# Optimization experiments

Hardware: AMD Instinct MI355X
Metric: run time of the kernel (lower is better)

## Reference

```python
import jax, jax.numpy as jnp
import numpy as np

B, S, E, H = 2, 2048, 768, 8
D = E // H  # 96
SCALING = D ** (-0.5)


def setup_inputs() -> dict:
    key = jax.random.key(0)
    ks = jax.random.split(key, 7)
    sd = E ** -0.5
    return {
        "x": jax.random.normal(ks[0], (B, S, E), jnp.float32),
        "Wq": jax.random.normal(ks[1], (E, E), jnp.float32) * sd,
        "bq": jax.random.normal(ks[2], (E,), jnp.float32) * 0.02,
        "Wk": jax.random.normal(ks[3], (E, E), jnp.float32) * sd,
        "bk": jax.random.normal(ks[4], (E,), jnp.float32) * 0.02,
        "Wo": jax.random.normal(ks[5], (E, E), jnp.float32) * sd,
        "bo": jax.random.normal(ks[6], (E,), jnp.float32) * 0.02,
    }


def _split_heads(t):
    # [B, S, E] -> [B, H, S, D]
    return t.reshape(B, S, H, D).transpose(0, 2, 1, 3)


def reference(x, Wq, bq, Wk, bk, Wo, bo):
    q = _split_heads(x @ Wq + bq)
    k = _split_heads(x @ Wk + bk)
    # NOTE: faithful to source bug — values use the KEY projection
    v = _split_heads(x @ Wk + bk)
    energies = jnp.einsum("bhqd,bhkd->bhqk", q, k)  # [B,H,S,S]
    # NOTE: faithful to source — scaling applied AFTER softmax
    attn = jax.nn.softmax(energies, axis=-1) * SCALING
    out = jnp.einsum("bhqk,bhkd->bhqd", attn, v)
    out = out.transpose(0, 2, 1, 3).reshape(B, S, E)
    return out @ Wo + bo
```

## Files before the change

kernel.cpp:

```cpp
#include <hip/hip_runtime.h>
#include <hip/hip_bf16.h>
#include <math.h>
#include <stdint.h>

#define B_DIM 2
#define S_DIM 2048
#define E_DIM 768
#define H_DIM 8
#define D_DIM 96
#define M_DIM (B_DIM*S_DIM)
#define SCALE_F 0.10206207261596575f
#define LOG2E_F 1.44269504088896341f

typedef _Float16 f16x8 __attribute__((ext_vector_type(8)));
typedef float    f32x4  __attribute__((ext_vector_type(4)));
typedef float    f32x16 __attribute__((ext_vector_type(16)));
typedef unsigned int u32x4 __attribute__((ext_vector_type(4)));

#define MFMA16H(a,b,c) __builtin_amdgcn_mfma_f32_16x16x32_f16(a,b,c,0,0,0)
#define MFMA32H(a,b,c) __builtin_amdgcn_mfma_f32_32x32x16_f16(a,b,c,0,0,0)

__device__ inline unsigned short f2h(float f) {
    return __builtin_bit_cast(unsigned short, (_Float16)f);
}

__device__ inline unsigned pk2(float a, float b) {
    return __builtin_bit_cast(unsigned, __builtin_amdgcn_cvt_pkrtz(a, b));
}

__device__ inline void gload16(const void* g, void* l) {
    auto gp = reinterpret_cast<const __attribute__((address_space(1))) uint32_t*>(
        reinterpret_cast<uintptr_t>(g));
    auto lp = reinterpret_cast<__attribute__((address_space(3))) uint32_t*>(
        reinterpret_cast<uintptr_t>(l));
    __builtin_amdgcn_global_load_lds(gp, lp, 16, 0, 0);
}

__global__ __launch_bounds__(256) void prep_kernel(
    const float* __restrict__ X,
    const float* __restrict__ W0, const float* __restrict__ W1,
    const float* __restrict__ W2,
    unsigned short* __restrict__ Xf,
    unsigned short* __restrict__ T0, unsigned short* __restrict__ T1,
    unsigned short* __restrict__ T2)
{
    const int tid = threadIdx.x;
    if (blockIdx.x < 3072) {
        int i = (blockIdx.x * 256 + tid) * 4;
        float4 v = *(const float4*)(X + i);
        ushort4 h;
        h.x = f2h(v.x); h.y = f2h(v.y); h.z = f2h(v.z); h.w = f2h(v.w);
        *(ushort4*)(Xf + i) = h;
        return;
    }
    int idx = blockIdx.x - 3072;
    int z = idx / 144, rem = idx % 144;
    const float* W; unsigned short* T;
    if (z == 0)      { W = W0; T = T0; }
    else if (z == 1) { W = W1; T = T1; }
    else             { W = W2; T = T2; }
    const float sc = (z == 0) ? LOG2E_F : 1.0f;
    int k0 = (rem / 12) << 6, n0 = (rem % 12) << 6;

    __shared__ float tile[64][65];
    const int r = tid >> 4, c4 = (tid & 15) << 2;
    #pragma unroll
    for (int i = 0; i < 4; ++i) {
        float4 v = *(const float4*)(W + (size_t)(k0 + r + i*16)*E_DIM + n0 + c4);
        tile[r + i*16][c4+0] = v.x; tile[r + i*16][c4+1] = v.y;
        tile[r + i*16][c4+2] = v.z; tile[r + i*16][c4+3] = v.w;
    }
    __syncthreads();
    #pragma unroll
    for (int i = 0; i < 4; ++i) {
        int n = r + i*16;
        ushort4 h;
        h.x = f2h(tile[c4+0][n] * sc); h.y = f2h(tile[c4+1][n] * sc);
        h.z = f2h(tile[c4+2][n] * sc); h.w = f2h(tile[c4+3][n] * sc);
        *(ushort4*)(T + (size_t)(n0 + n)*E_DIM + k0 + c4) = h;
    }
}

__global__ __launch_bounds__(256) void gemm_qk_kernel(
    const unsigned short* __restrict__ A, const unsigned short* __restrict__ Bt,
    const float* __restrict__ bq, const float* __restrict__ bk,
    unsigned short* __restrict__ Qf, unsigned short* __restrict__ Kf)
{
    __shared__ unsigned short sA[2*128*32];
    __shared__ unsigned short sB[2*64*32];

    const int tid  = threadIdx.x;
    const int lane = tid & 63;
    const int w    = tid >> 6;
    const int qn   = lane & 15, quad = lane >> 4;
    const int wm   = w & 1, wn = w >> 1;

    const int flat = blockIdx.x;
    const int g = flat & 7, s = flat >> 3;
    const int row0 = ((g << 2) + (s & 3)) << 7;
    const int col0 = (s >> 2) << 6;

    const int ar = tid >> 2;
    const int ak = (tid & 3) << 3;

    const unsigned short* gA = A  + (size_t)(row0 + ar)*E_DIM + ak;
    const unsigned short* gB = Bt + (size_t)(col0 + ar)*E_DIM + ak;

    f32x4 acc[4][2];
    #pragma unroll
    for (int mt = 0; mt < 4; ++mt)
        #pragma unroll
        for (int nt = 0; nt < 2; ++nt)
            { acc[mt][nt][0]=0.f; acc[mt][nt][1]=0.f; acc[mt][nt][2]=0.f; acc[mt][nt][3]=0.f; }

    for (int k0 = 0; k0 < E_DIM; k0 += 64) {
        __syncthreads();
        gload16(gA + k0,                 sA + tid*8);
        gload16(gA + 64*E_DIM + k0,      sA + 2048 + tid*8);
        gload16(gA + k0 + 32,            sA + 4096 + tid*8);
        gload16(gA + 64*E_DIM + k0 + 32, sA + 6144 + tid*8);
        gload16(gB + k0,                 sB + tid*8);
        gload16(gB + k0 + 32,            sB + 2048 + tid*8);
        __syncthreads();

        #pragma unroll
        for (int kk = 0; kk < 2; ++kk) {
            f16x8 af[4], bf[2];
            #pragma unroll
            for (int mt = 0; mt < 4; ++mt)
                af[mt] = *(const f16x8*)&sA[kk*4096 + (wm*64 + mt*16 + qn)*32 + quad*8];
            #pragma unroll
            for (int nt = 0; nt < 2; ++nt)
                bf[nt] = *(const f16x8*)&sB[kk*2048 + (wn*32 + nt*16 + qn)*32 + quad*8];
            #pragma unroll
            for (int mt = 0; mt < 4; ++mt)
                #pragma unroll
                for (int nt = 0; nt < 2; ++nt)
                    acc[mt][nt] = MFMA16H(af[mt], bf[nt], acc[mt][nt]);
        }
    }

    #pragma unroll
    for (int nt = 0; nt < 2; ++nt) {
        int n = col0 + wn*32 + nt*16 + qn;
        bool isQ = n < E_DIM;
        float bias = isQ ? bq[n] * LOG2E_F : bk[n - E_DIM];
        unsigned short* op = isQ ? Qf : Kf;
        int nc = isQ ? n : n - E_DIM;
        #pragma unroll
        for (int mt = 0; mt < 4; ++mt)
            #pragma unroll
            for (int r = 0; r < 4; ++r) {
                int m = row0 + wm*64 + mt*16 + quad*4 + r;
                op[(size_t)m*E_DIM + nc] = f2h(acc[mt][nt][r] + bias);
            }
    }
}

__global__ __launch_bounds__(128, 2) void attn_mfma_kernel(
    const unsigned short* __restrict__ Qf, const unsigned short* __restrict__ Kf,
    unsigned short* __restrict__ O0, unsigned short* __restrict__ O1,
    unsigned short* __restrict__ O2, unsigned short* __restrict__ O3,
    float2* __restrict__ ml)
{
    __shared__ unsigned short sKh[64][104];
    __shared__ unsigned short sKt[96][72];

    const int tid  = threadIdx.x;
    const int w    = tid >> 6;
    const int lane = tid & 63;
    const int col  = lane & 31;
    const int half = lane >> 5;
    const int b    = blockIdx.z >> 2;
    const int ks   = blockIdx.z & 3;
    const int h    = blockIdx.y;
    const int q0   = blockIdx.x << 7;
    const int key0 = ks << 9;

    f16x8 qf[2][6];
    #pragma unroll
    for (int qb = 0; qb < 2; ++qb) {
        const size_t ro = ((size_t)(b*S_DIM + q0 + w*64 + qb*32 + col))*E_DIM
                          + h*D_DIM + half*8;
        #pragma unroll
        for (int kc = 0; kc < 6; ++kc)
            qf[qb][kc] = *(const f16x8*)(Qf + ro + kc*16);
    }

    f32x16 o[2][3];
    #pragma unroll
    for (int qb = 0; qb < 2; ++qb)
        #pragma unroll
        for (int nt = 0; nt < 3; ++nt)
            #pragma unroll
            for (int r = 0; r < 16; ++r) o[qb][nt][r] = 0.f;
    float m_i[2] = {-INFINITY, -INFINITY};
    float l_i[2] = {0.f, 0.f};

    const int sp = tid >> 2;
    const int dq = tid & 3;
    const int kp2 = ((sp + ((dq & 1) << 4)) & 31) << 1;

    uint4 r0[3], r1[3];
    {
        const size_t g0 = ((size_t)(b*S_DIM + key0 + 2*sp))*E_DIM + h*D_DIM + dq*8;
        #pragma unroll
        for (int i = 0; i < 3; ++i) {
            r0[i] = *(const uint4*)(Kf + g0 + 32*i);
            r1[i] = *(const uint4*)(Kf + g0 + E_DIM + 32*i);
        }
    }

    const int kswz = ((col >> 3) & 1) << 2;

    for (int kt = 0; kt < 8; ++kt) {
        {
            #pragma unroll
            for (int i = 0; i < 3; ++i) {
                *(uint4*)&sKh[2*sp  ][dq*8 + 32*i] = r0[i];
                *(uint4*)&sKh[2*sp+1][dq*8 + 32*i] = r1[i];
            }
            const unsigned short* p0 = (const unsigned short*)r0;
            const unsigned short* p1 = (const unsigned short*)r1;
            #pragma unroll
            for (int c = 0; c < 24; ++c) {
                int d = dq*8 + ((c >> 3) << 5) + (c & 7);
                unsigned pk = (unsigned)p0[c] | ((unsigned)p1[c] << 16);
                *(unsigned*)&sKt[d][kp2] = pk;
            }
        }
        __syncthreads();

        if (kt + 1 < 8) {
            const size_t g0 = ((size_t)(b*S_DIM + key0 + (kt+1)*64 + 2*sp))*E_DIM
                              + h*D_DIM + dq*8;
            #pragma unroll
            for (int i = 0; i < 3; ++i) {
                r0[i] = *(const uint4*)(Kf + g0 + 32*i);
                r1[i] = *(const uint4*)(Kf + g0 + E_DIM + 32*i);
            }
        }

        f32x16 s[2][2];
        #pragma unroll
        for (int qb = 0; qb < 2; ++qb)
            #pragma unroll
            for (int mt = 0; mt < 2; ++mt)
                #pragma unroll
                for (int r = 0; r < 16; ++r) s[qb][mt][r] = 0.f;
        #pragma unroll
        for (int mt = 0; mt < 2; ++mt)
            #pragma unroll
            for (int kc = 0; kc < 6; ++kc) {
                f16x8 ah = *(const f16x8*)&sKh[mt*32 + col][kc*16 + half*8];
                s[0][mt] = MFMA32H(ah, qf[0][kc], s[0][mt]);
                s[1][mt] = MFMA32H(ah, qf[1][kc], s[1][mt]);
            }

        #pragma unroll
        for (int qb = 0; qb < 2; ++qb) {
            float t[8];
            #pragma unroll
            for (int r = 0; r < 8; ++r)
                t[r] = fmaxf(fmaxf(s[qb][0][r], s[qb][0][r+8]),
                             fmaxf(s[qb][1][r], s[qb][1][r+8]));
            float mx = fmaxf(fmaxf(fmaxf(t[0], t[1]), fmaxf(t[2], t[3])),
                             fmaxf(fmaxf(t[4], t[5]), fmaxf(t[6], t[7])));
            mx = fmaxf(mx, __shfl_xor(mx, 32));

            if (__any(mx > m_i[qb] + 10.0f)) {
                float m_new = fmaxf(m_i[qb], mx);
                float alpha = __builtin_amdgcn_exp2f(m_i[qb] - m_new);
                l_i[qb] *= alpha;
                #pragma unroll
                for (int nt = 0; nt < 3; ++nt)
                    #pragma unroll
                    for (int r = 0; r < 16; ++r) o[qb][nt][r] *= alpha;
                m_i[qb] = m_new;
            }

            #pragma unroll
            for (int mt = 0; mt < 2; ++mt)
                #pragma unroll
                for (int r = 0; r < 16; ++r)
                    s[qb][mt][r] = __builtin_amdgcn_exp2f(s[qb][mt][r] - m_i[qb]);

            float a[8];
            #pragma unroll
            for (int r = 0; r < 8; ++r)
                a[r] = (s[qb][0][r] + s[qb][0][r+8]) + (s[qb][1][r] + s[qb][1][r+8]);
            float ps = ((a[0]+a[1]) + (a[2]+a[3])) + ((a[4]+a[5]) + (a[6]+a[7]));
            ps += __shfl_xor(ps, 32);
            l_i[qb] += ps;
        }

        #pragma unroll
        for (int kc = 0; kc < 4; ++kc) {
            const int mt = kc >> 1;
            const int g0 = (kc & 1) << 3;
            f16x8 pb[2];
            #pragma unroll
            for (int qb = 0; qb < 2; ++qb) {
                unsigned A0 = pk2(s[qb][mt][g0+0], s[qb][mt][g0+1]);
                unsigned A1 = pk2(s[qb][mt][g0+2], s[qb][mt][g0+3]);
                unsigned B0 = pk2(s[qb][mt][g0+4], s[qb][mt][g0+5]);
                unsigned B1 = pk2(s[qb][mt][g0+6], s[qb][mt][g0+7]);
                auto w0 = __builtin_amdgcn_permlane32_swap(A0, B0, false, false);
                auto w1 = __builtin_amdgcn_permlane32_swap(A1, B1, false, false);
                u32x4 pw;
                pw[0] = w0[0]; pw[1] = w1[0]; pw[2] = w0[1]; pw[3] = w1[1];
                pb[qb] = __builtin_bit_cast(f16x8, pw);
            }
            #pragma unroll
            for (int nt = 0; nt < 3; ++nt) {
                f16x8 va = *(const f16x8*)
                    &sKt[nt*32 + col][(((kc << 1) | half) ^ kswz) << 3];
                o[0][nt] = MFMA32H(va, pb[0], o[0][nt]);
                o[1][nt] = MFMA32H(va, pb[1], o[1][nt]);
            }
        }
        __syncthreads();
    }

    unsigned short* Obase = O0;
    if (ks == 1) Obase = O1; else if (ks == 2) Obase = O2; else if (ks == 3) Obase = O3;
    #pragma unroll
    for (int qb = 0; qb < 2; ++qb) {
        float inv = 1.0f / l_i[qb];
        unsigned short* Ob = Obase
            + ((size_t)(b*S_DIM + q0 + w*64 + qb*32 + col))*E_DIM + h*D_DIM;
        #pragma unroll
        for (int nt = 0; nt < 3; ++nt)
            #pragma unroll
            for (int rg = 0; rg < 4; ++rg) {
                ushort4 pk;
                pk.x = f2h(o[qb][nt][4*rg+0]*inv); pk.y = f2h(o[qb][nt][4*rg+1]*inv);
                pk.z = f2h(o[qb][nt][4*rg+2]*inv); pk.w = f2h(o[qb][nt][4*rg+3]*inv);
                *(ushort4*)(Ob + nt*32 + 8*rg + 4*half) = pk;
            }
    }
    if (lane < 32) {
        #pragma unroll
        for (int qb = 0; qb < 2; ++qb) {
            int q = q0 + w*64 + qb*32 + lane;
            ml[((size_t)(ks*B_DIM + b)*H_DIM + h)*S_DIM + q]
                = make_float2(m_i[qb], l_i[qb]);
        }
    }
}

__device__ inline float4 mkscale4(const float2* __restrict__ ml, int m, int h) {
    int b = m >> 11, q = m & (S_DIM - 1);
    float2 e0 = ml[((size_t)(0*B_DIM + b)*H_DIM + h)*S_DIM + q];
    float2 e1 = ml[((size_t)(1*B_DIM + b)*H_DIM + h)*S_DIM + q];
    float2 e2 = ml[((size_t)(2*B_DIM + b)*H_DIM + h)*S_DIM + q];
    float2 e3 = ml[((size_t)(3*B_DIM + b)*H_DIM + h)*S_DIM + q];
    float mm = fmaxf(fmaxf(e0.x, e1.x), fmaxf(e2.x, e3.x));
    float w0 = e0.y * __builtin_amdgcn_exp2f(e0.x - mm);
    float w1 = e1.y * __builtin_amdgcn_exp2f(e1.x - mm);
    float w2 = e2.y * __builtin_amdgcn_exp2f(e2.x - mm);
    float w3 = e3.y * __builtin_amdgcn_exp2f(e3.x - mm);
    float inv = SCALE_F / (w0 + w1 + w2 + w3);
    return make_float4(w0*inv, w1*inv, w2*inv, w3*inv);
}

__global__ __launch_bounds__(256) void gemm_out_kernel(
    const unsigned short* __restrict__ O0, const unsigned short* __restrict__ O1,
    const unsigned short* __restrict__ O2, const unsigned short* __restrict__ O3,
    const float2* __restrict__ ml, const unsigned short* __restrict__ Bt,
    const float* __restrict__ bo, float* __restrict__ out)
{
    __shared__ unsigned short sA[2*64*32];
    __shared__ unsigned short sB[2*64*32];

    const int tid  = threadIdx.x;
    const int lane = tid & 63;
    const int w    = tid >> 6;
    const int qn   = lane & 15, quad = lane >> 4;
    const int wm   = w & 1, wn = w >> 1;

    const int flat = blockIdx.x;
    const int g = flat & 7, s = flat >> 3;
    const int row0 = ((g << 3) + (s & 7)) << 6;
    const int col0 = (s >> 3) << 6;

    const int ar = tid >> 2;
    const int ak = (tid & 3) << 3;

    const size_t r0o = (size_t)(row0 + ar)*E_DIM;
    const unsigned short* gB = Bt + (size_t)(col0 + ar)*E_DIM + ak;

    f32x4 acc[2][2];
    #pragma unroll
    for (int mt = 0; mt < 2; ++mt)
        #pragma unroll
        for (int nt = 0; nt < 2; ++nt)
            { acc[mt][nt][0]=0.f; acc[mt][nt][1]=0.f; acc[mt][nt][2]=0.f; acc[mt][nt][3]=0.f; }

    f16x8 u0A = *(const f16x8*)(O0 + r0o + ak);
    f16x8 u1A = *(const f16x8*)(O1 + r0o + ak);
    f16x8 u2A = *(const f16x8*)(O2 + r0o + ak);
    f16x8 u3A = *(const f16x8*)(O3 + r0o + ak);
    f16x8 u0B = *(const f16x8*)(O0 + r0o + 32 + ak);
    f16x8 u1B = *(const f16x8*)(O1 + r0o + 32 + ak);
    f16x8 u2B = *(const f16x8*)(O2 + r0o + 32 + ak);
    f16x8 u3B = *(const f16x8*)(O3 + r0o + 32 + ak);
    int hA = 0, hB = 0;
    float4 s4 = mkscale4(ml, row0 + ar, 0);
    _Float16 aA0 = (_Float16)s4.x, aA1 = (_Float16)s4.y;
    _Float16 aA2 = (_Float16)s4.z, aA3 = (_Float16)s4.w;
    _Float16 aB0 = aA0, aB1 = aA1, aB2 = aA2, aB3 = aA3;

    for (int k0 = 0; k0 < E_DIM; k0 += 64) {
        __syncthreads();
        {
            f16x8 c0 = (u0A*aA0 + u1A*aA1) + (u2A*aA2 + u3A*aA3);
            f16x8 c1 = (u0B*aB0 + u1B*aB1) + (u2B*aB2 + u3B*aB3);
            *(f16x8*)&sA[       ar*32 + ak] = c0;
            *(f16x8*)&sA[2048 + ar*32 + ak] = c1;
        }
        gload16(gB + k0,      sB + tid*8);
        gload16(gB + k0 + 32, sB + 2048 + tid*8);
        __syncthreads();

        if (k0 + 64 < E_DIM) {
            int kn = k0 + 64;
            u0A = *(const f16x8*)(O0 + r0o + kn + ak);
            u1A = *(const f16x8*)(O1 + r0o + kn + ak);
            u2A = *(const f16x8*)(O2 + r0o + kn + ak);
            u3A = *(const f16x8*)(O3 + r0o + kn + ak);
            u0B = *(const f16x8*)(O0 + r0o + kn + 32 + ak);
            u1B = *(const f16x8*)(O1 + r0o + kn + 32 + ak);
            u2B = *(const f16x8*)(O2 + r0o + kn + 32 + ak);
            u3B = *(const f16x8*)(O3 + r0o + kn + 32 + ak);
            int nhA = kn / D_DIM, nhB = (kn + 32) / D_DIM;
            if (nhA != hA) {
                float4 t4 = mkscale4(ml, row0 + ar, nhA);
                aA0 = (_Float16)t4.x; aA1 = (_Float16)t4.y;
                aA2 = (_Float16)t4.z; aA3 = (_Float16)t4.w; hA = nhA;
            }
            if (nhB != hB) {
                float4 t4 = mkscale4(ml, row0 + ar, nhB);
                aB0 = (_Float16)t4.x; aB1 = (_Float16)t4.y;
                aB2 = (_Float16)t4.z; aB3 = (_Float16)t4.w; hB = nhB;
            }
        }

        #pragma unroll
        for (int kk = 0; kk < 2; ++kk) {
            f16x8 af[2], bf[2];
            #pragma unroll
            for (int mt = 0; mt < 2; ++mt)
                af[mt] = *(const f16x8*)&sA[kk*2048 + (wm*32 + mt*16 + qn)*32 + quad*8];
            #pragma unroll
            for (int nt = 0; nt < 2; ++nt)
                bf[nt] = *(const f16x8*)&sB[kk*2048 + (wn*32 + nt*16 + qn)*32 + quad*8];
            #pragma unroll
            for (int mt = 0; mt < 2; ++mt)
                #pragma unroll
                for (int nt = 0; nt < 2; ++nt)
                    acc[mt][nt] = MFMA16H(af[mt], bf[nt], acc[mt][nt]);
        }
    }

    #pragma unroll
    for (int nt = 0; nt < 2; ++nt) {
        int n = col0 + wn*32 + nt*16 + qn;
        float bias = bo[n];
        #pragma unroll
        for (int mt = 0; mt < 2; ++mt)
            #pragma unroll
            for (int r = 0; r < 4; ++r) {
                int m = row0 + wm*32 + mt*16 + quad*4 + r;
                out[(size_t)m*E_DIM + n] = acc[mt][nt][r] + bias;
            }
    }
}

extern "C" void kernel_launch(void* const* d_in, const int* in_sizes, int n_in,
                              void* d_out, int out_size, void* d_ws, size_t ws_size,
                              hipStream_t stream)
{
    const float* x  = (const float*)d_in[0];
    const float* Wq = (const float*)d_in[1];
    const float* bq = (const float*)d_in[2];
    const float* Wk = (const float*)d_in[3];
    const float* bk = (const float*)d_in[4];
    const float* Wo = (const float*)d_in[5];
    const float* bo = (const float*)d_in[6];
    float* out = (float*)d_out;

    const size_t NE = (size_t)M_DIM * E_DIM;
    const size_t WE = (size_t)E_DIM * E_DIM;
    unsigned short* xf    = (unsigned short*)d_ws;
    unsigned short* WqkT  = xf + NE;
    unsigned short* WoT   = WqkT + 2*WE;
    unsigned short* Qf    = WoT + WE;
    unsigned short* Kf    = Qf + NE;
    unsigned short* Oh1   = Kf + NE;
    unsigned short* Oh2   = Oh1 + NE;
    unsigned short* Oh3   = Oh2 + NE;
    float2*         mlbuf = (float2*)(Oh3 + NE);
    unsigned short* Oh0   = xf;

    dim3 blk(256);
    hipLaunchKernelGGL(prep_kernel, dim3(3504), blk, 0, stream,
                       x, Wq, Wk, Wo, xf, WqkT, WqkT + WE, WoT);

    hipLaunchKernelGGL(gemm_qk_kernel, dim3(768), blk, 0, stream,
                       xf, WqkT, bq, bk, Qf, Kf);

    hipLaunchKernelGGL(attn_mfma_kernel, dim3(S_DIM/128, H_DIM, B_DIM*4),
                       dim3(128), 0, stream, Qf, Kf, Oh0, Oh1, Oh2, Oh3, mlbuf);

    hipLaunchKernelGGL(gemm_out_kernel, dim3(768), blk, 0, stream,
                       Oh0, Oh1, Oh2, Oh3, mlbuf, WoT, bo, out);
}
```

Baseline: 162.2 us.

## Enlarge GEMM tiles and split split-K combine into a separate kernel

The QK projection GEMM now uses 128x128 tiles instead of 128x64, halving the grid and raising per-block reuse of the A and B tiles. The output GEMM no longer merges the four partial attention outputs inline. A new combine kernel writes the merged fp16 activation to a buffer reusing Qf, and the output GEMM then runs as a plain 128x64-tile GEMM. This adds an extra launch and a round trip through global memory for the merged tensor. The larger tiles raise register use and cut the number of blocks.

```diff
diff --git a/kernel.cpp b/kernel.cpp
--- a/kernel.cpp
+++ b/kernel.cpp
@@ -87,7 +87,7 @@
     unsigned short* __restrict__ Qf, unsigned short* __restrict__ Kf)
 {
     __shared__ unsigned short sA[2*128*32];
-    __shared__ unsigned short sB[2*64*32];
+    __shared__ unsigned short sB[2*128*32];
 
     const int tid  = threadIdx.x;
     const int lane = tid & 63;
@@ -98,7 +98,7 @@
     const int flat = blockIdx.x;
     const int g = flat & 7, s = flat >> 3;
     const int row0 = ((g << 2) + (s & 3)) << 7;
-    const int col0 = (s >> 2) << 6;
+    const int col0 = (s >> 2) << 7;
 
     const int ar = tid >> 2;
     const int ak = (tid & 3) << 3;
@@ -106,11 +106,11 @@
     const unsigned short* gA = A  + (size_t)(row0 + ar)*E_DIM + ak;
     const unsigned short* gB = Bt + (size_t)(col0 + ar)*E_DIM + ak;
 
-    f32x4 acc[4][2];
+    f32x4 acc[4][4];
     #pragma unroll
     for (int mt = 0; mt < 4; ++mt)
         #pragma unroll
-        for (int nt = 0; nt < 2; ++nt)
+        for (int nt = 0; nt < 4; ++nt)
             { acc[mt][nt][0]=0.f; acc[mt][nt][1]=0.f; acc[mt][nt][2]=0.f; acc[mt][nt][3]=0.f; }
 
     for (int k0 = 0; k0 < E_DIM; k0 += 64) {
@@ -120,29 +120,31 @@
         gload16(gA + k0 + 32,            sA + 4096 + tid*8);
         gload16(gA + 64*E_DIM + k0 + 32, sA + 6144 + tid*8);
         gload16(gB + k0,                 sB + tid*8);
-        gload16(gB + k0 + 32,            sB + 2048 + tid*8);
+        gload16(gB + 64*E_DIM + k0,      sB + 2048 + tid*8);
+        gload16(gB + k0 + 32,            sB + 4096 + tid*8);
+        gload16(gB + 64*E_DIM + k0 + 32, sB + 6144 + tid*8);
         __syncthreads();
 
         #pragma unroll
         for (int kk = 0; kk < 2; ++kk) {
-            f16x8 af[4], bf[2];
+            f16x8 af[4], bf[4];
             #pragma unroll
             for (int mt = 0; mt < 4; ++mt)
                 af[mt] = *(const f16x8*)&sA[kk*4096 + (wm*64 + mt*16 + qn)*32 + quad*8];
             #pragma unroll
-            for (int nt = 0; nt < 2; ++nt)
-                bf[nt] = *(const f16x8*)&sB[kk*2048 + (wn*32 + nt*16 + qn)*32 + quad*8];
+            for (int nt = 0; nt < 4; ++nt)
+                bf[nt] = *(const f16x8*)&sB[kk*4096 + (wn*64 + nt*16 + qn)*32 + quad*8];
             #pragma unroll
             for (int mt = 0; mt < 4; ++mt)
                 #pragma unroll
-                for (int nt = 0; nt < 2; ++nt)
+                for (int nt = 0; nt < 4; ++nt)
                     acc[mt][nt] = MFMA16H(af[mt], bf[nt], acc[mt][nt]);
         }
     }
 
     #pragma unroll
-    for (int nt = 0; nt < 2; ++nt) {
-        int n = col0 + wn*32 + nt*16 + qn;
+    for (int nt = 0; nt < 4; ++nt) {
+        int n = col0 + wn*64 + nt*16 + qn;
         bool isQ = n < E_DIM;
         float bias = isQ ? bq[n] * LOG2E_F : bk[n - E_DIM];
         unsigned short* op = isQ ? Qf : Kf;
@@ -364,13 +366,29 @@
     return make_float4(w0*inv, w1*inv, w2*inv, w3*inv);
 }
 
-__global__ __launch_bounds__(256) void gemm_out_kernel(
+__global__ __launch_bounds__(256) void combine_kernel(
     const unsigned short* __restrict__ O0, const unsigned short* __restrict__ O1,
     const unsigned short* __restrict__ O2, const unsigned short* __restrict__ O3,
-    const float2* __restrict__ ml, const unsigned short* __restrict__ Bt,
+    const float2* __restrict__ ml, unsigned short* __restrict__ Oc)
+{
+    const int idx = (blockIdx.x * 256 + threadIdx.x) * 8;
+    const int m = idx / E_DIM, col = idx % E_DIM;
+    const int h = col / D_DIM;
+    float4 s4 = mkscale4(ml, m, h);
+    f16x8 u0 = *(const f16x8*)(O0 + idx);
+    f16x8 u1 = *(const f16x8*)(O1 + idx);
+    f16x8 u2 = *(const f16x8*)(O2 + idx);
+    f16x8 u3 = *(const f16x8*)(O3 + idx);
+    f16x8 c = (u0*(_Float16)s4.x + u1*(_Float16)s4.y)
+            + (u2*(_Float16)s4.z + u3*(_Float16)s4.w);
+    *(f16x8*)(Oc + idx) = c;
+}
+
+__global__ __launch_bounds__(256) void gemm_out_kernel(
+    const unsigned short* __restrict__ A, const unsigned short* __restrict__ Bt,
     const float* __restrict__ bo, float* __restrict__ out)
 {
-    __shared__ unsigned short sA[2*64*32];
+    __shared__ unsigned short sA[2*128*32];
     __shared__ unsigned short sB[2*64*32];
 
     const int tid  = threadIdx.x;
@@ -381,82 +399,43 @@
 
     const int flat = blockIdx.x;
     const int g = flat & 7, s = flat >> 3;
-    const int row0 = ((g << 3) + (s & 7)) << 6;
-    const int col0 = (s >> 3) << 6;
+    const int row0 = ((g << 2) + (s & 3)) << 7;
+    const int col0 = (s >> 2) << 6;
 
     const int ar = tid >> 2;
     const int ak = (tid & 3) << 3;
 
-    const size_t r0o = (size_t)(row0 + ar)*E_DIM;
+    const unsigned short* gA = A  + (size_t)(row0 + ar)*E_DIM + ak;
     const unsigned short* gB = Bt + (size_t)(col0 + ar)*E_DIM + ak;
 
-    f32x4 acc[2][2];
-    #pragma unroll
-    for (int mt = 0; mt < 2; ++mt)
+    f32x4 acc[4][2];
+    #pragma unroll
+    for (int mt = 0; mt < 4; ++mt)
         #pragma unroll
         for (int nt = 0; nt < 2; ++nt)
             { acc[mt][nt][0]=0.f; acc[mt][nt][1]=0.f; acc[mt][nt][2]=0.f; acc[mt][nt][3]=0.f; }
 
-    f16x8 u0A = *(const f16x8*)(O0 + r0o + ak);
-    f16x8 u1A = *(const f16x8*)(O1 + r0o + ak);
-    f16x8 u2A = *(const f16x8*)(O2 + r0o + ak);
-    f16x8 u3A = *(const f16x8*)(O3 + r0o + ak);
-    f16x8 u0B = *(const f16x8*)(O0 + r0o + 32 + ak);
-    f16x8 u1B = *(const f16x8*)(O1 + r0o + 32 + ak);
-    f16x8 u2B = *(const f16x8*)(O2 + r0o + 32 + ak);
-    f16x8 u3B = *(const f16x8*)(O3 + r0o + 32 + ak);
-    int hA = 0, hB = 0;
-    float4 s4 = mkscale4(ml, row0 + ar, 0);
-    _Float16 aA0 = (_Float16)s4.x, aA1 = (_Float16)s4.y;
-    _Float16 aA2 = (_Float16)s4.z, aA3 = (_Float16)s4.w;
-    _Float16 aB0 = aA0, aB1 = aA1, aB2 = aA2, aB3 = aA3;
-
     for (int k0 = 0; k0 < E_DIM; k0 += 64) {
         __syncthreads();
-        {
-            f16x8 c0 = (u0A*aA0 + u1A*aA1) + (u2A*aA2 + u3A*aA3);
-            f16x8 c1 = (u0B*aB0 + u1B*aB1) + (u2B*aB2 + u3B*aB3);
-            *(f16x8*)&sA[       ar*32 + ak] = c0;
-            *(f16x8*)&sA[2048 + ar*32 + ak] = c1;
-        }
-        gload16(gB + k0,      sB + tid*8);
-        gload16(gB + k0 + 32, sB + 2048 + tid*8);
+        gload16(gA + k0,                 sA + tid*8);
+        gload16(gA + 64*E_DIM + k0,      sA + 2048 + tid*8);
+        gload16(gA + k0 + 32,            sA + 4096 + tid*8);
+        gload16(gA + 64*E_DIM + k0 + 32, sA + 6144 + tid*8);
+        gload16(gB + k0,                 sB + tid*8);
+        gload16(gB + k0 + 32,            sB + 2048 + tid*8);
         __syncthreads();
 
-        if (k0 + 64 < E_DIM) {
-            int kn = k0 + 64;
-            u0A = *(const f16x8*)(O0 + r0o + kn + ak);
-            u1A = *(const f16x8*)(O1 + r0o + kn + ak);
-            u2A = *(const f16x8*)(O2 + r0o + kn + ak);
-            u3A = *(const f16x8*)(O3 + r0o + kn + ak);
-            u0B = *(const f16x8*)(O0 + r0o + kn + 32 + ak);
-            u1B = *(const f16x8*)(O1 + r0o + kn + 32 + ak);
-            u2B = *(const f16x8*)(O2 + r0o + kn + 32 + ak);
-            u3B = *(const f16x8*)(O3 + r0o + kn + 32 + ak);
-            int nhA = kn / D_DIM, nhB = (kn + 32) / D_DIM;
-            if (nhA != hA) {
-                float4 t4 = mkscale4(ml, row0 + ar, nhA);
-                aA0 = (_Float16)t4.x; aA1 = (_Float16)t4.y;
-                aA2 = (_Float16)t4.z; aA3 = (_Float16)t4.w; hA = nhA;
-            }
-            if (nhB != hB) {
-                float4 t4 = mkscale4(ml, row0 + ar, nhB);
-                aB0 = (_Float16)t4.x; aB1 = (_Float16)t4.y;
-                aB2 = (_Float16)t4.z; aB3 = (_Float16)t4.w; hB = nhB;
-            }
-        }
-
         #pragma unroll
         for (int kk = 0; kk < 2; ++kk) {
-            f16x8 af[2], bf[2];
-            #pragma unroll
-            for (int mt = 0; mt < 2; ++mt)
-                af[mt] = *(const f16x8*)&sA[kk*2048 + (wm*32 + mt*16 + qn)*32 + quad*8];
+            f16x8 af[4], bf[2];
+            #pragma unroll
+            for (int mt = 0; mt < 4; ++mt)
+                af[mt] = *(const f16x8*)&sA[kk*4096 + (wm*64 + mt*16 + qn)*32 + quad*8];
             #pragma unroll
             for (int nt = 0; nt < 2; ++nt)
                 bf[nt] = *(const f16x8*)&sB[kk*2048 + (wn*32 + nt*16 + qn)*32 + quad*8];
             #pragma unroll
-            for (int mt = 0; mt < 2; ++mt)
+            for (int mt = 0; mt < 4; ++mt)
                 #pragma unroll
                 for (int nt = 0; nt < 2; ++nt)
                     acc[mt][nt] = MFMA16H(af[mt], bf[nt], acc[mt][nt]);
@@ -468,10 +447,10 @@
         int n = col0 + wn*32 + nt*16 + qn;
         float bias = bo[n];
         #pragma unroll
-        for (int mt = 0; mt < 2; ++mt)
+        for (int mt = 0; mt < 4; ++mt)
             #pragma unroll
             for (int r = 0; r < 4; ++r) {
-                int m = row0 + wm*32 + mt*16 + quad*4 + r;
+                int m = row0 + wm*64 + mt*16 + quad*4 + r;
                 out[(size_t)m*E_DIM + n] = acc[mt][nt][r] + bias;
             }
     }
@@ -502,17 +481,21 @@
     unsigned short* Oh3   = Oh2 + NE;
     float2*         mlbuf = (float2*)(Oh3 + NE);
     unsigned short* Oh0   = xf;
+    unsigned short* Oc    = Qf;
 
     dim3 blk(256);
     hipLaunchKernelGGL(prep_kernel, dim3(3504), blk, 0, stream,
                        x, Wq, Wk, Wo, xf, WqkT, WqkT + WE, WoT);
 
-    hipLaunchKernelGGL(gemm_qk_kernel, dim3(768), blk, 0, stream,
+    hipLaunchKernelGGL(gemm_qk_kernel, dim3(384), blk, 0, stream,
                        xf, WqkT, bq, bk, Qf, Kf);
 
     hipLaunchKernelGGL(attn_mfma_kernel, dim3(S_DIM/128, H_DIM, B_DIM*4),
                        dim3(128), 0, stream, Qf, Kf, Oh0, Oh1, Oh2, Oh3, mlbuf);
 
-    hipLaunchKernelGGL(gemm_out_kernel, dim3(768), blk, 0, stream,
-                       Oh0, Oh1, Oh2, Oh3, mlbuf, WoT, bo, out);
-}
+    hipLaunchKernelGGL(combine_kernel, dim3((M_DIM*E_DIM)/(256*8)), blk, 0,
+                       stream, Oh0, Oh1, Oh2, Oh3, mlbuf, Oc);
+
+    hipLaunchKernelGGL(gemm_out_kernel, dim3(384), blk, 0, stream,
+                       Oc, WoT, bo, out);
+}
```

Result: no change. 159.7 us (-1.5%).
